# Optimization experiments

Measured on AMD Instinct MI355X. Metric: run time of the kernel, lower is better.

The kernel has to match this reference:

```python
import jax, jax.numpy as jnp
import numpy as np

C = 128          # hidden width hard-coded in DirModelToFace
EPS = 1e-5       # BatchNorm1d eps


def sparse_bmm(rows, cols, vals, x, num_rows):
    """Batched sparse @ dense: COO (rows, cols, vals) shared across batch.
    x: [B, K, c] -> [B, num_rows, c]."""
    def one(xb):
        return jax.ops.segment_sum(xb[cols] * vals[:, None], rows, num_segments=num_rows)
    return jax.vmap(one)(x)


def conv1x1_prebn(x, gamma, beta, W, b):
    # GraphConv1x1(batch_norm='pre'): BN (training stats over B*N rows) then Linear
    mean = x.mean((0, 1))
    var = x.var((0, 1))  # biased, as torch BN uses for normalization
    xh = (x - mean) * jax.lax.rsqrt(var + EPS) * gamma + beta
    return xh @ W + b


def dir_block(Di, DiA, v, f, g, be, W, b):
    # DirResNet2 (res_f=False): quaternionic Dirac message passing
    B, N, _ = v.shape
    Fn = f.shape[1]
    msg_v = sparse_bmm(*DiA, f.reshape(B, 4 * Fn, C // 4), 4 * N).reshape(B, N, C)
    x = jax.nn.elu(jnp.concatenate([v, msg_v], axis=-1))
    v_out = v + conv1x1_prebn(x, g[0], be[0], W[0], b[0])
    msg_f = sparse_bmm(*Di, v_out.reshape(B, 4 * N, C // 4), 4 * Fn).reshape(B, Fn, C)
    x = jax.nn.elu(jnp.concatenate([f, msg_f], axis=-1))
    f_out = conv1x1_prebn(x, g[1], be[1], W[1], b[1])  # no residual on f
    return v_out, f_out


def avg_block(mask, v, g, be, W, b):
    # AvgResNet2: masked global average message
    x = v
    for j in range(2):
        x = jax.nn.elu(x)
        x_avg = (mask * x).sum(1, keepdims=True) / mask.sum(1, keepdims=True)
        x = jnp.concatenate([x, jnp.broadcast_to(x_avg, x.shape)], axis=-1)
        x = conv1x1_prebn(x, g[j], be[j], W[j], b[j])
    return x + v


def setup_inputs() -> dict:
    key = jax.random.key(0)
    ks = jax.random.split(key, 10)
    B, N, Fn = 4, 12000, 24000
    nnz = 48 * Fn  # 3 vertices per face x 4x4 quaternion block
    inputs = jax.random.normal(ks[0], (B, N, 3), jnp.float32)
    mask = jnp.ones((B, N, 1), jnp.float32)
    Di_rows = jax.random.randint(ks[1], (nnz,), 0, 4 * Fn, jnp.int32)
    Di_cols = jax.random.randint(ks[2], (nnz,), 0, 4 * N, jnp.int32)
    Di_vals = jax.random.normal(ks[3], (nnz,), jnp.float32) * 0.1
    DiA_rows = jax.random.randint(ks[4], (nnz,), 0, 4 * N, jnp.int32)
    DiA_cols = jax.random.randint(ks[5], (nnz,), 0, 4 * Fn, jnp.int32)
    DiA_vals = jax.random.normal(ks[6], (nnz,), jnp.float32) * 0.1
    W1 = jax.random.normal(ks[7], (3, C), jnp.float32) / np.sqrt(3.0)
    b1 = jnp.zeros((C,), jnp.float32)
    rn_gamma = jnp.ones((16, 2, 2 * C), jnp.float32)
    rn_beta = jnp.zeros((16, 2, 2 * C), jnp.float32)
    rn_W = jax.random.normal(ks[8], (16, 2, 2 * C, C), jnp.float32) / np.sqrt(2.0 * C)
    rn_b = jnp.zeros((16, 2, C), jnp.float32)
    g2 = jnp.ones((C,), jnp.float32)
    be2 = jnp.zeros((C,), jnp.float32)
    W2 = jax.random.normal(ks[9], (C, 1), jnp.float32) / np.sqrt(1.0 * C)
    b2 = jnp.zeros((1,), jnp.float32)
    return dict(inputs=inputs, mask=mask,
                Di_rows=Di_rows, Di_cols=Di_cols, Di_vals=Di_vals,
                DiA_rows=DiA_rows, DiA_cols=DiA_cols, DiA_vals=DiA_vals,
                W1=W1, b1=b1, rn_gamma=rn_gamma, rn_beta=rn_beta, rn_W=rn_W, rn_b=rn_b,
                g2=g2, be2=be2, W2=W2, b2=b2, num_faces=24000)


def reference(inputs, mask, Di_rows, Di_cols, Di_vals, DiA_rows, DiA_cols, DiA_vals,
              W1, b1, rn_gamma, rn_beta, rn_W, rn_b, g2, be2, W2, b2, num_faces):
    B, N, _ = inputs.shape
    v = inputs @ W1 + b1                       # conv1 (batch_norm=None)
    f = jnp.zeros((B, num_faces, C), v.dtype)  # face features start at zero
    Di = (Di_rows, Di_cols, Di_vals)
    DiA = (DiA_rows, DiA_cols, DiA_vals)
    for i in range(16):
        if i % 2 == 0:
            v, f = dir_block(Di, DiA, v, f, rn_gamma[i], rn_beta[i], rn_W[i], rn_b[i])
        else:
            v = avg_block(mask, v, rn_gamma[i], rn_beta[i], rn_W[i], rn_b[i])
    x = jax.nn.elu(f)
    return conv1x1_prebn(x, g2, be2, W2, b2)   # conv2 (batch_norm='pre')
```

## Files before the change

kernel.cpp:

```cpp
#include <hip/hip_runtime.h>
#include <hip/hip_fp16.h>
#include <math.h>


#define EPS 1e-5f

typedef float floatx4 __attribute__((ext_vector_type(4)));
typedef short shortx8 __attribute__((ext_vector_type(8)));

__device__ __forceinline__ float eluf(float x) { return x > 0.f ? x : expm1f(x); }
__device__ __forceinline__ float4 elu4(float4 v) {
    v.x = eluf(v.x); v.y = eluf(v.y); v.z = eluf(v.z); v.w = eluf(v.w); return v;
}
__device__ __forceinline__ short f2bf(float x) {
    unsigned u = __builtin_bit_cast(unsigned, x);
    u = u + 0x7FFFu + ((u >> 16) & 1u);
    return (short)(u >> 16);
}
__device__ __forceinline__ float bf2f(short h) {
    unsigned u = ((unsigned)(unsigned short)h) << 16;
    return __builtin_bit_cast(float, u);
}
__device__ __forceinline__ void split2(float x, short& hi, short& lo) {
    unsigned u = __builtin_bit_cast(unsigned, x);
    hi = (short)(u >> 16);
    float r = x - bf2f(hi);
    lo = (short)(__builtin_bit_cast(unsigned, r) >> 16);
}

__global__ void conv1_kernel(const float* __restrict__ in, const float* __restrict__ W1,
                             const float* __restrict__ b1, float* __restrict__ v,
                             __half* __restrict__ vH, int N, float* __restrict__ Sout) {
    int t = threadIdx.x;
    int c = t & 127, half = t >> 7;
    int r0 = blockIdx.x * 64;
    float w0 = W1[c], w1 = W1[128 + c], w2 = W1[256 + c], bb = b1[c];
    float s1 = 0.f, s2 = 0.f;
    for (int k = 0; k < 32; ++k) {
        int r = r0 + half + 2 * k;
        float x0 = in[r * 3 + 0], x1 = in[r * 3 + 1], x2 = in[r * 3 + 2];
        float val = bb + x0 * w0 + x1 * w1 + x2 * w2;
        v[(size_t)r * 128 + c] = val;
        int b = r / N, vert = r - b * N;
        vH[(size_t)(4 * vert + (c >> 5)) * 128 + b * 32 + (c & 31)] = __float2half(val);
        float e = eluf(val);
        s1 += e; s2 += e * e;
    }
    atomicAdd(&Sout[c], s1);
    atomicAdd(&Sout[256 + c], s2);
}

__global__ void masksum_kernel(const float* __restrict__ mask, float* __restrict__ msum,
                               int N) {
    int b = blockIdx.x, t = threadIdx.x;
    float s = 0.f;
    for (int n = t; n < N; n += 256) s += mask[(size_t)b * N + n];
    for (int o = 32; o > 0; o >>= 1) s += __shfl_down(s, o);
    __shared__ float sh[4];
    if ((t & 63) == 0) sh[t >> 6] = s;
    __syncthreads();
    if (t == 0) msum[b] = sh[0] + sh[1] + sh[2] + sh[3];
}


__global__ void hist_kernel(const int* __restrict__ rows, int* __restrict__ counts) {
    int e = blockIdx.x * 256 + threadIdx.x;
    atomicAdd(&counts[rows[e]], 1);
}

__global__ void partial_kernel(const int* __restrict__ counts, int* __restrict__ partials,
                               int R) {
    int t = threadIdx.x;
    int base = blockIdx.x * 1024 + t * 4;
    int s = 0;
#pragma unroll
    for (int j = 0; j < 4; ++j) { int i = base + j; if (i < R) s += counts[i]; }
    __shared__ int sh[256];
    sh[t] = s; __syncthreads();
    for (int st = 128; st > 0; st >>= 1) {
        if (t < st) sh[t] += sh[t + st];
        __syncthreads();
    }
    if (t == 0) partials[blockIdx.x] = sh[0];
}

__global__ void scanp_kernel(int* __restrict__ partials, int* __restrict__ rowptr,
                             int P, int R, int total) {
    __shared__ int sh[256];
    int t = threadIdx.x;
    int v = (t < P) ? partials[t] : 0;
    sh[t] = v; __syncthreads();
    for (int st = 1; st < 256; st <<= 1) {
        int tmp = (t >= st) ? sh[t - st] : 0;
        __syncthreads();
        sh[t] += tmp;
        __syncthreads();
    }
    if (t < P) partials[t] = sh[t] - v;
    if (t == 0) rowptr[R] = total;
}

__global__ void apply_kernel(int* __restrict__ counts, const int* __restrict__ partials,
                             int* __restrict__ rowptr, int R) {
    int t = threadIdx.x;
    int base = blockIdx.x * 1024 + t * 4;
    int c[4]; int s = 0;
#pragma unroll
    for (int j = 0; j < 4; ++j) { int i = base + j; c[j] = (i < R) ? counts[i] : 0; s += c[j]; }
    __shared__ int sh[256];
    sh[t] = s; __syncthreads();
    for (int st = 1; st < 256; st <<= 1) {
        int tmp = (t >= st) ? sh[t - st] : 0;
        __syncthreads();
        sh[t] += tmp;
        __syncthreads();
    }
    int off = partials[blockIdx.x] + sh[t] - s;
#pragma unroll
    for (int j = 0; j < 4; ++j) {
        int i = base + j;
        if (i < R) { rowptr[i] = off; counts[i] = off; }
        off += c[j];
    }
}

__global__ void scatter_kernel(const int* __restrict__ rows, const int* __restrict__ cols,
                               const float* __restrict__ vals, int* __restrict__ fill,
                               int2* __restrict__ edges) {
    int e = blockIdx.x * 256 + threadIdx.x;
    int p = atomicAdd(&fill[rows[e]], 1);
    edges[p] = make_int2(cols[e], __float_as_int(vals[e]));
}

__global__ __launch_bounds__(1024) void spmm_csr_kernel(
    const int* __restrict__ rowptr, const int2* __restrict__ edges,
    const __half2* __restrict__ xH, float* __restrict__ y, int R4,
    float* __restrict__ Sout) {
    int t = threadIdx.x;
    int waveId = blockIdx.x * 16 + (t >> 6);
    int lane = t & 63;
    int b = lane >> 4, cp = lane & 15;
    const __half2* xb = xH + b * 16 + cp;
    size_t rs = (size_t)R4 * 32;
    __shared__ float red[256];
    if (t < 256) red[t] = 0.f;
    __syncthreads();
#pragma unroll
    for (int rr = 0; rr < 2; ++rr) {
        int r = waveId * 2 + rr;
        int e0 = rowptr[r], e1 = rowptr[r + 1];
        float ax = 0.f, ay = 0.f;
        int e = e0;
        for (; e + 4 <= e1; e += 4) {
            int2 E0 = edges[e], E1 = edges[e + 1], E2 = edges[e + 2], E3 = edges[e + 3];
            __half2 g0 = xb[(size_t)E0.x * 64];
            __half2 g1 = xb[(size_t)E1.x * 64];
            __half2 g2 = xb[(size_t)E2.x * 64];
            __half2 g3 = xb[(size_t)E3.x * 64];
            float v0 = __int_as_float(E0.y), v1 = __int_as_float(E1.y);
            float v2 = __int_as_float(E2.y), v3 = __int_as_float(E3.y);
            float2 f0 = __half22float2(g0), f1 = __half22float2(g1);
            float2 f2 = __half22float2(g2), f3 = __half22float2(g3);
            ax += v0 * f0.x; ay += v0 * f0.y;
            ax += v1 * f1.x; ay += v1 * f1.y;
            ax += v2 * f2.x; ay += v2 * f2.y;
            ax += v3 * f3.x; ay += v3 * f3.y;
        }
        for (; e < e1; ++e) {
            int2 E = edges[e];
            __half2 g = xb[(size_t)E.x * 64];
            float v = __int_as_float(E.y);
            float2 f = __half22float2(g);
            ax += v * f.x; ay += v * f.y;
        }
        *(float2*)&y[(size_t)b * rs + (size_t)r * 32 + cp * 2] = make_float2(ax, ay);
        float ea = eluf(ax), eb = eluf(ay);
        float s1a = ea, s2a = ea * ea, s1b = eb, s2b = eb * eb;
        s1a += __shfl_xor(s1a, 16); s1a += __shfl_xor(s1a, 32);
        s2a += __shfl_xor(s2a, 16); s2a += __shfl_xor(s2a, 32);
        s1b += __shfl_xor(s1b, 16); s1b += __shfl_xor(s1b, 32);
        s2b += __shfl_xor(s2b, 16); s2b += __shfl_xor(s2b, 32);
        if (lane < 16) {
            int ch = (r & 3) * 32 + cp * 2;
            atomicAdd(&red[ch], s1a);
            atomicAdd(&red[ch + 1], s1b);
            atomicAdd(&red[128 + ch], s2a);
            atomicAdd(&red[128 + ch + 1], s2b);
        }
    }
    __syncthreads();
    if (t < 128) atomicAdd(&Sout[128 + t], red[t]);
    else if (t < 256) atomicAdd(&Sout[384 + (t - 128)], red[t]);
}

__global__ void fold_kernel(const float* __restrict__ S, const float* __restrict__ gamma,
                            const float* __restrict__ beta, const float* __restrict__ W,
                            const float* __restrict__ bvec, short* __restrict__ Wh,
                            short* __restrict__ Wl, float* __restrict__ bp, float invR) {
    __shared__ float red[256];
    int o = blockIdx.x, k = threadIdx.x;
    float mean = S[k] * invR;
    float var = S[256 + k] * invR - mean * mean;
    float s = gamma[k] / sqrtf(var + EPS);
    float w = W[(size_t)k * 128 + o];
    float wp = s * w;
    short h = f2bf(wp);
    Wh[(size_t)o * 256 + k] = h;
    Wl[(size_t)o * 256 + k] = f2bf(wp - bf2f(h));
    red[k] = (beta[k] - mean * s) * w;
    __syncthreads();
    for (int st = 128; st > 0; st >>= 1) {
        if (k < st) red[k] += red[k + st];
        __syncthreads();
    }
    if (k == 0) bp[o] = bvec[o] + red[0];
}

__global__ __launch_bounds__(256) void gemm_mfma(
    const float* __restrict__ A, const float* __restrict__ Bs,
    const short* __restrict__ Wh, const short* __restrict__ Wl,
    const float* __restrict__ bp, const float* __restrict__ resid,
    float* __restrict__ out, __half* __restrict__ shadow,
    float* __restrict__ Sout, const float* __restrict__ mask,
    float* __restrict__ avgout, int rowsPerBatch, int modeB, int eluB) {
    __shared__ short Bsh[128 * 40];
    __shared__ short Bsl[128 * 40];
    const int t = threadIdx.x;
    const int lane = t & 63;
    const int wave = t >> 6;
    const int rowBase = blockIdx.x * 128 + wave * 32;
    const int m = lane & 15;
    const int kq = lane >> 4;
    floatx4 acc[2][8];
#pragma unroll
    for (int i = 0; i < 2; ++i)
#pragma unroll
        for (int j = 0; j < 8; ++j) acc[i][j] = {0.f, 0.f, 0.f, 0.f};

    const int kbEnd = (modeB == 2) ? 4 : 8;
    for (int kb = 0; kb < kbEnd; ++kb) {
        const int k0 = kb * 32 + kq * 8;
        __syncthreads();
#pragma unroll
        for (int i = 0; i < 2; ++i) {
            int idx = t + 256 * i;
            int col = idx >> 2, q = idx & 3;
            shortx8 h = *(const shortx8*)&Wh[(size_t)col * 256 + kb * 32 + q * 8];
            shortx8 l = *(const shortx8*)&Wl[(size_t)col * 256 + kb * 32 + q * 8];
            *(shortx8*)&Bsh[col * 40 + q * 8] = h;
            *(shortx8*)&Bsl[col * 40 + q * 8] = l;
        }
        shortx8 ah[2], al[2];
#pragma unroll
        for (int rg = 0; rg < 2; ++rg) {
            int row = rowBase + rg * 16 + m;
            float4 p, q;
            if (kb < 4) {
                p = elu4(*(const float4*)&A[(size_t)row * 128 + k0]);
                q = elu4(*(const float4*)&A[(size_t)row * 128 + k0 + 4]);
            } else {
                int kk = k0 - 128;
                if (modeB == 0) {
                    p = *(const float4*)&Bs[(size_t)row * 128 + kk];
                    q = *(const float4*)&Bs[(size_t)row * 128 + kk + 4];
                    if (eluB) { p = elu4(p); q = elu4(q); }
                } else {
                    int b = row / rowsPerBatch;
                    p = *(const float4*)&Bs[b * 128 + kk];
                    q = *(const float4*)&Bs[b * 128 + kk + 4];
                }
            }
            float x[8] = {p.x, p.y, p.z, p.w, q.x, q.y, q.z, q.w};
#pragma unroll
            for (int j = 0; j < 8; ++j) {
                short h, l;
                split2(x[j], h, l);
                ah[rg][j] = h;
                al[rg][j] = l;
            }
        }
        __syncthreads();
#pragma unroll
        for (int ct = 0; ct < 8; ++ct) {
            int co = (ct * 16 + m) * 40 + kq * 8;
            shortx8 bh = *(const shortx8*)&Bsh[co];
            shortx8 bl = *(const shortx8*)&Bsl[co];
#pragma unroll
            for (int rg = 0; rg < 2; ++rg) {
                acc[rg][ct] = __builtin_amdgcn_mfma_f32_16x16x32_bf16(ah[rg], bh, acc[rg][ct], 0, 0, 0);
                acc[rg][ct] = __builtin_amdgcn_mfma_f32_16x16x32_bf16(ah[rg], bl, acc[rg][ct], 0, 0, 0);
                acc[rg][ct] = __builtin_amdgcn_mfma_f32_16x16x32_bf16(al[rg], bh, acc[rg][ct], 0, 0, 0);
            }
        }
    }
    const int bBlk = (blockIdx.x * 128) / rowsPerBatch;
    float mk8[8]; int ib8[8];
    if (avgout) {
#pragma unroll
        for (int rg = 0; rg < 2; ++rg)
#pragma unroll
            for (int r = 0; r < 4; ++r) {
                int row = rowBase + rg * 16 + kq * 4 + r;
                mk8[rg * 4 + r] = mask[row];
                ib8[rg * 4 + r] = (row >= (bBlk + 1) * rowsPerBatch) ? 1 : 0;
            }
    }
    float cs1[8], cs2[8], av0[8], av1[8];
#pragma unroll
    for (int ct = 0; ct < 8; ++ct) { cs1[ct] = 0.f; cs2[ct] = 0.f; av0[ct] = 0.f; av1[ct] = 0.f; }
#pragma unroll
    for (int ct = 0; ct < 8; ++ct) {
        int col = ct * 16 + m;
        float bb = bp[col];
#pragma unroll
        for (int rg = 0; rg < 2; ++rg) {
#pragma unroll
            for (int r = 0; r < 4; ++r) {
                int row = rowBase + rg * 16 + kq * 4 + r;
                size_t o = (size_t)row * 128 + col;
                float v = acc[rg][ct][r] + bb;
                if (resid) v += resid[o];
                out[o] = v;
                if (shadow) {
                    int b = row / rowsPerBatch, vert = row - b * rowsPerBatch;
                    shadow[(size_t)(4 * vert + (col >> 5)) * 128 + b * 32 + (col & 31)] =
                        __float2half(v);
                }
                float e = eluf(v);
                cs1[ct] += e; cs2[ct] += e * e;
                if (avgout) {
                    float me = mk8[rg * 4 + r] * e;
                    if (ib8[rg * 4 + r]) av1[ct] += me; else av0[ct] += me;
                }
            }
        }
    }
    if (Sout) {
        __syncthreads();
        float* red = (float*)Bsh;
        float* redv = (float*)Bsl;
        red[t] = 0.f;
        if (avgout) redv[t] = 0.f;
        __syncthreads();
#pragma unroll
        for (int ct = 0; ct < 8; ++ct) {
            cs1[ct] += __shfl_xor(cs1[ct], 16); cs1[ct] += __shfl_xor(cs1[ct], 32);
            cs2[ct] += __shfl_xor(cs2[ct], 16); cs2[ct] += __shfl_xor(cs2[ct], 32);
            if (avgout) {
                av0[ct] += __shfl_xor(av0[ct], 16); av0[ct] += __shfl_xor(av0[ct], 32);
                av1[ct] += __shfl_xor(av1[ct], 16); av1[ct] += __shfl_xor(av1[ct], 32);
            }
        }
        if (kq == 0) {
#pragma unroll
            for (int ct = 0; ct < 8; ++ct) {
                atomicAdd(&red[ct * 16 + m], cs1[ct]);
                atomicAdd(&red[128 + ct * 16 + m], cs2[ct]);
                if (avgout) {
                    atomicAdd(&redv[ct * 16 + m], av0[ct]);
                    atomicAdd(&redv[128 + ct * 16 + m], av1[ct]);
                }
            }
        }
        __syncthreads();
        if (t < 128) atomicAdd(&Sout[t], red[t]);
        else atomicAdd(&Sout[256 + (t - 128)], red[t]);
        if (avgout) {
            int plane = t >> 7, col = t & 127;
            int b = bBlk + plane;
            if (b < 4) atomicAdd(&avgout[b * 128 + col], redv[t]);
        }
    }
}

__global__ void finalize_avg(const float* __restrict__ avgacc, const float* __restrict__ masksum,
                             float* __restrict__ avg, float* __restrict__ S, float fN) {
    int c = threadIdx.x;
    float s1 = 0.f, s2 = 0.f;
    for (int b = 0; b < 4; ++b) {
        float a = avgacc[b * 128 + c] / masksum[b];
        avg[b * 128 + c] = a;
        s1 += a; s2 += a * a;
    }
    S[128 + c] = s1 * fN;
    S[256 + 128 + c] = s2 * fN;
}

__global__ void fold_final(const float* __restrict__ S, const float* __restrict__ g2,
                           const float* __restrict__ be2, const float* __restrict__ W2,
                           const float* __restrict__ b2, float* __restrict__ W2p, float invR) {
    __shared__ float red[128];
    int c = threadIdx.x;
    float mean = S[c] * invR;
    float var = S[256 + c] * invR - mean * mean;
    float s = g2[c] / sqrtf(var + EPS);
    float w = W2[c];
    W2p[c] = s * w;
    red[c] = (be2[c] - mean * s) * w;
    __syncthreads();
    for (int st = 64; st > 0; st >>= 1) {
        if (c < st) red[c] += red[c + st];
        __syncthreads();
    }
    if (c == 0) W2p[128] = b2[0] + red[0];
}

__global__ void final_out_kernel(const float* __restrict__ f, const float* __restrict__ W2p,
                                 float* __restrict__ out) {
    int t = threadIdx.x;
    int w = t >> 6, lane = t & 63;
    int row = blockIdx.x * 4 + w;
    float a = eluf(f[(size_t)row * 128 + lane]) * W2p[lane] +
              eluf(f[(size_t)row * 128 + 64 + lane]) * W2p[64 + lane];
    for (int off = 32; off > 0; off >>= 1) a += __shfl_down(a, off);
    if (lane == 0) out[row] = a + W2p[128];
}

extern "C" void kernel_launch(void* const* d_in, const int* in_sizes, int n_in,
                              void* d_out, int out_size, void* d_ws, size_t ws_size,
                              hipStream_t stream) {
    const float* inputs = (const float*)d_in[0];
    const float* mask = (const float*)d_in[1];
    const int* Di_rows = (const int*)d_in[2];
    const int* Di_cols = (const int*)d_in[3];
    const float* Di_vals = (const float*)d_in[4];
    const int* DiA_rows = (const int*)d_in[5];
    const int* DiA_cols = (const int*)d_in[6];
    const float* DiA_vals = (const float*)d_in[7];
    const float* W1 = (const float*)d_in[8];
    const float* b1 = (const float*)d_in[9];
    const float* rn_gamma = (const float*)d_in[10];
    const float* rn_beta = (const float*)d_in[11];
    const float* rn_W = (const float*)d_in[12];
    const float* rn_b = (const float*)d_in[13];
    const float* g2 = (const float*)d_in[14];
    const float* be2 = (const float*)d_in[15];
    const float* W2 = (const float*)d_in[16];
    const float* b2 = (const float*)d_in[17];
    float* out = (float*)d_out;

    const int B = 4;
    const int BN = in_sizes[1];
    const int N = BN / B;
    const int BF = out_size;
    const int Fn = BF / B;
    const int nnz = in_sizes[2];
    const int RA = 4 * N;
    const int RD = 4 * Fn;

    float* ws = (float*)d_ws;
    size_t off = 0;
    float* vA = ws + off;  off += (size_t)BN * 128;
    float* fA = ws + off;  off += (size_t)BF * 128;
    float* msg = ws + off; off += (size_t)BF * 128;
    __half* vH = (__half*)(ws + off); off += (size_t)RA * 128 / 2;
    __half* fH = (__half*)(ws + off); off += (size_t)RD * 128 / 2;
    int* ptrA    = (int*)(ws + off);  off += (size_t)RA + 4;
    int2* edgesA = (int2*)(ws + off); off += (size_t)nnz * 2;
    int* ptrD    = (int*)(ws + off);  off += (size_t)RD + 4;
    int2* edgesD = (int2*)(ws + off); off += (size_t)nnz * 2;
    int* tmpfill = (int*)(ws + off);  off += (size_t)RD;
    int* partials = (int*)(ws + off); off += 256;
    float* Sarena = ws + off; off += 33 * 512;
    float* Aarena = ws + off; off += 16 * 512;
    float* msum = ws + off;   off += 4;
    float* avg = ws + off;    off += 512;
    short* Wh = (short*)(ws + off); off += 128 * 256 / 2;
    short* Wl = (short*)(ws + off); off += 128 * 256 / 2;
    float* bp = ws + off;  off += 128;
    float* W2p = ws + off; off += 132;

    const int eBlocks = nnz / 256;
    const int PA = (RA + 1023) / 1024;
    const int PD = (RD + 1023) / 1024;

    hipMemsetAsync(Sarena, 0, (33 * 512 + 16 * 512) * 4, stream);
    hipMemsetAsync(fA, 0, (size_t)BF * 128 * 4, stream);

    hipMemsetAsync(tmpfill, 0, (size_t)RA * 4, stream);
    hist_kernel<<<eBlocks, 256, 0, stream>>>(DiA_rows, tmpfill);
    partial_kernel<<<PA, 256, 0, stream>>>(tmpfill, partials, RA);
    scanp_kernel<<<1, 256, 0, stream>>>(partials, ptrA, PA, RA, nnz);
    apply_kernel<<<PA, 256, 0, stream>>>(tmpfill, partials, ptrA, RA);
    scatter_kernel<<<eBlocks, 256, 0, stream>>>(DiA_rows, DiA_cols, DiA_vals, tmpfill, edgesA);
    hipMemsetAsync(tmpfill, 0, (size_t)RD * 4, stream);
    hist_kernel<<<eBlocks, 256, 0, stream>>>(Di_rows, tmpfill);
    partial_kernel<<<PD, 256, 0, stream>>>(tmpfill, partials, RD);
    scanp_kernel<<<1, 256, 0, stream>>>(partials, ptrD, PD, RD, nnz);
    apply_kernel<<<PD, 256, 0, stream>>>(tmpfill, partials, ptrD, RD);
    scatter_kernel<<<eBlocks, 256, 0, stream>>>(Di_rows, Di_cols, Di_vals, tmpfill, edgesD);

    auto slot = [&](int i, int j) { return Sarena + 512 * (2 * i + j); };
    float* Sfinal = Sarena + 512 * 32;

    masksum_kernel<<<B, 256, 0, stream>>>(mask, msum, N);
    conv1_kernel<<<BN / 64, 256, 0, stream>>>(inputs, W1, b1, vA, vH, N, slot(0, 0));

    for (int i = 0; i < 15; ++i) {
        if ((i & 1) == 0) {
            const float* g0 = rn_gamma + (size_t)(i * 2 + 0) * 256;
            const float* be0 = rn_beta + (size_t)(i * 2 + 0) * 256;
            const float* Wl0 = rn_W + (size_t)(i * 2 + 0) * 256 * 128;
            const float* bl0 = rn_b + (size_t)(i * 2 + 0) * 128;
            const float* g1 = rn_gamma + (size_t)(i * 2 + 1) * 256;
            const float* be1 = rn_beta + (size_t)(i * 2 + 1) * 256;
            const float* Wl1 = rn_W + (size_t)(i * 2 + 1) * 256 * 128;
            const float* bl1 = rn_b + (size_t)(i * 2 + 1) * 128;
            float* SoutV = (i < 14) ? slot(i + 1, 0) : nullptr;
            float* avgV = (i < 14) ? (Aarena + 512 * i) : nullptr;

            if (i == 0) {
                fold_kernel<<<128, 256, 0, stream>>>(slot(0, 0), g0, be0, Wl0, bl0,
                                                     Wh, Wl, bp, 1.f / BN);
                gemm_mfma<<<BN / 128, 256, 0, stream>>>(vA, nullptr, Wh, Wl, bp, vA, vA,
                                                        vH, SoutV, mask, avgV, N, 2, 1);
            } else {
                spmm_csr_kernel<<<RA / 32, 1024, 0, stream>>>(ptrA, edgesA,
                                                              (const __half2*)fH, msg, RA,
                                                              slot(i, 0));
                fold_kernel<<<128, 256, 0, stream>>>(slot(i, 0), g0, be0, Wl0, bl0,
                                                     Wh, Wl, bp, 1.f / BN);
                gemm_mfma<<<BN / 128, 256, 0, stream>>>(vA, msg, Wh, Wl, bp, vA, vA,
                                                        vH, SoutV, mask, avgV, N, 0, 1);
            }

            spmm_csr_kernel<<<RD / 32, 1024, 0, stream>>>(ptrD, edgesD, (const __half2*)vH,
                                                          msg, RD, slot(i, 1));
            fold_kernel<<<128, 256, 0, stream>>>(slot(i, 1), g1, be1, Wl1, bl1, Wh, Wl,
                                                 bp, 1.f / BF);
            gemm_mfma<<<BF / 128, 256, 0, stream>>>(fA, msg, Wh, Wl, bp, nullptr, fA, fH,
                                                    (i < 14) ? slot(i + 2, 1) : Sfinal,
                                                    nullptr, nullptr, Fn, 0, 1);
        } else {
            for (int j = 0; j < 2; ++j) {
                const float* g = rn_gamma + (size_t)(i * 2 + j) * 256;
                const float* be = rn_beta + (size_t)(i * 2 + j) * 256;
                const float* Wlw = rn_W + (size_t)(i * 2 + j) * 256 * 128;
                const float* bl = rn_b + (size_t)(i * 2 + j) * 128;
                const float* src = (j == 0) ? vA : msg;
                float* dst = (j == 0) ? msg : vA;
                const float* resid = (j == 0) ? nullptr : vA;
                __half* shadow = (j == 0) ? nullptr : vH;
                float* Sout = (j == 0) ? slot(i, 1) : slot(i + 1, 0);
                float* avgO = (j == 0) ? (Aarena + 512 * i) : nullptr;

                float* avgacc = Aarena + 512 * (i - 1 + j);
                finalize_avg<<<1, 128, 0, stream>>>(avgacc, msum, avg, slot(i, j),
                                                    (float)N);
                fold_kernel<<<128, 256, 0, stream>>>(slot(i, j), g, be, Wlw, bl, Wh, Wl,
                                                     bp, 1.f / BN);
                gemm_mfma<<<BN / 128, 256, 0, stream>>>(src, avg, Wh, Wl, bp, resid, dst,
                                                        shadow, Sout, mask, avgO, N, 1, 0);
            }
        }
    }

    fold_final<<<1, 128, 0, stream>>>(Sfinal, g2, be2, W2, b2, W2p, 1.f / BF);
    final_out_kernel<<<BF / 4, 256, 0, stream>>>(fA, W2p, out);
}
```

Measured before the change: 4.195 ms.

## Store SpMM messages in fp16 and process two K-blocks per GEMM sync

The SpMM kernel now writes its message output as fp16 with nontemporal stores and reads edges with nontemporal loads. The BN statistics are computed from the rounded fp16 values so they match what the GEMM consumes. The GEMM decodes the fp16 message operand and stages two 32-wide K slices of weights in shared memory per barrier pair, halving the number of synchronizations. This cuts message write and read traffic and barrier overhead, at the cost of fp16 rounding on messages, more LDS and more registers, plus a separate fp32 scratch buffer for the average blocks.

```diff
diff --git a/kernel.cpp b/kernel.cpp
--- a/kernel.cpp
+++ b/kernel.cpp
@@ -7,6 +7,8 @@
 
 typedef float floatx4 __attribute__((ext_vector_type(4)));
 typedef short shortx8 __attribute__((ext_vector_type(8)));
+typedef int intx2 __attribute__((ext_vector_type(2)));
+typedef int intx4 __attribute__((ext_vector_type(4)));
 
 __device__ __forceinline__ float eluf(float x) { return x > 0.f ? x : expm1f(x); }
 __device__ __forceinline__ float4 elu4(float4 v) {
@@ -26,6 +28,9 @@
     hi = (short)(u >> 16);
     float r = x - bf2f(hi);
     lo = (short)(__builtin_bit_cast(unsigned, r) >> 16);
+}
+__device__ __forceinline__ float2 h2f(int bits) {
+    return __half22float2(__builtin_bit_cast(__half2, bits));
 }
 
 __global__ void conv1_kernel(const float* __restrict__ in, const float* __restrict__ W1,
@@ -134,13 +139,14 @@
 
 __global__ __launch_bounds__(1024) void spmm_csr_kernel(
     const int* __restrict__ rowptr, const int2* __restrict__ edges,
-    const __half2* __restrict__ xH, float* __restrict__ y, int R4,
+    const __half2* __restrict__ xH, __half* __restrict__ yH, int R4,
     float* __restrict__ Sout) {
     int t = threadIdx.x;
     int waveId = blockIdx.x * 16 + (t >> 6);
     int lane = t & 63;
     int b = lane >> 4, cp = lane & 15;
     const __half2* xb = xH + b * 16 + cp;
+    const intx2* eg = (const intx2*)edges;
     size_t rs = (size_t)R4 * 32;
     __shared__ float red[256];
     if (t < 256) red[t] = 0.f;
@@ -152,7 +158,10 @@
         float ax = 0.f, ay = 0.f;
         int e = e0;
         for (; e + 4 <= e1; e += 4) {
-            int2 E0 = edges[e], E1 = edges[e + 1], E2 = edges[e + 2], E3 = edges[e + 3];
+            intx2 E0 = __builtin_nontemporal_load(&eg[e]);
+            intx2 E1 = __builtin_nontemporal_load(&eg[e + 1]);
+            intx2 E2 = __builtin_nontemporal_load(&eg[e + 2]);
+            intx2 E3 = __builtin_nontemporal_load(&eg[e + 3]);
             __half2 g0 = xb[(size_t)E0.x * 64];
             __half2 g1 = xb[(size_t)E1.x * 64];
             __half2 g2 = xb[(size_t)E2.x * 64];
@@ -167,14 +176,17 @@
             ax += v3 * f3.x; ay += v3 * f3.y;
         }
         for (; e < e1; ++e) {
-            int2 E = edges[e];
+            intx2 E = __builtin_nontemporal_load(&eg[e]);
             __half2 g = xb[(size_t)E.x * 64];
             float v = __int_as_float(E.y);
             float2 f = __half22float2(g);
             ax += v * f.x; ay += v * f.y;
         }
-        *(float2*)&y[(size_t)b * rs + (size_t)r * 32 + cp * 2] = make_float2(ax, ay);
-        float ea = eluf(ax), eb = eluf(ay);
+        __half2 hv = __floats2half2_rn(ax, ay);
+        __builtin_nontemporal_store(__builtin_bit_cast(int, hv),
+                                    (int*)(yH + (size_t)b * rs + (size_t)r * 32 + cp * 2));
+        float2 fv = __half22float2(hv);
+        float ea = eluf(fv.x), eb = eluf(fv.y);
         float s1a = ea, s2a = ea * ea, s1b = eb, s2b = eb * eb;
         s1a += __shfl_xor(s1a, 16); s1a += __shfl_xor(s1a, 32);
         s2a += __shfl_xor(s2a, 16); s2a += __shfl_xor(s2a, 32);
@@ -217,14 +229,15 @@
 }
 
 __global__ __launch_bounds__(256) void gemm_mfma(
-    const float* __restrict__ A, const float* __restrict__ Bs,
-    const short* __restrict__ Wh, const short* __restrict__ Wl,
-    const float* __restrict__ bp, const float* __restrict__ resid,
-    float* __restrict__ out, __half* __restrict__ shadow,
-    float* __restrict__ Sout, const float* __restrict__ mask,
-    float* __restrict__ avgout, int rowsPerBatch, int modeB, int eluB) {
-    __shared__ short Bsh[128 * 40];
-    __shared__ short Bsl[128 * 40];
+    const float* __restrict__ A, const __half* __restrict__ BsH,
+    const float* __restrict__ Bsf, const short* __restrict__ Wh,
+    const short* __restrict__ Wl, const float* __restrict__ bp,
+    const float* __restrict__ resid, float* __restrict__ out,
+    __half* __restrict__ shadow, float* __restrict__ Sout,
+    const float* __restrict__ mask, float* __restrict__ avgout,
+    int rowsPerBatch, int modeB, int eluB) {
+    __shared__ short Bh2[2][128 * 40];
+    __shared__ short Bl2[2][128 * 40];
     const int t = threadIdx.x;
     const int lane = t & 63;
     const int wave = t >> 6;
@@ -237,59 +250,72 @@
 #pragma unroll
         for (int j = 0; j < 8; ++j) acc[i][j] = {0.f, 0.f, 0.f, 0.f};
 
-    const int kbEnd = (modeB == 2) ? 4 : 8;
-    for (int kb = 0; kb < kbEnd; ++kb) {
-        const int k0 = kb * 32 + kq * 8;
-        __syncthreads();
-#pragma unroll
-        for (int i = 0; i < 2; ++i) {
-            int idx = t + 256 * i;
-            int col = idx >> 2, q = idx & 3;
-            shortx8 h = *(const shortx8*)&Wh[(size_t)col * 256 + kb * 32 + q * 8];
-            shortx8 l = *(const shortx8*)&Wl[(size_t)col * 256 + kb * 32 + q * 8];
-            *(shortx8*)&Bsh[col * 40 + q * 8] = h;
-            *(shortx8*)&Bsl[col * 40 + q * 8] = l;
-        }
-        shortx8 ah[2], al[2];
-#pragma unroll
-        for (int rg = 0; rg < 2; ++rg) {
-            int row = rowBase + rg * 16 + m;
-            float4 p, q;
-            if (kb < 4) {
-                p = elu4(*(const float4*)&A[(size_t)row * 128 + k0]);
-                q = elu4(*(const float4*)&A[(size_t)row * 128 + k0 + 4]);
-            } else {
-                int kk = k0 - 128;
-                if (modeB == 0) {
-                    p = *(const float4*)&Bs[(size_t)row * 128 + kk];
-                    q = *(const float4*)&Bs[(size_t)row * 128 + kk + 4];
-                    if (eluB) { p = elu4(p); q = elu4(q); }
+    const int kb2End = (modeB == 2) ? 2 : 4;
+    for (int kb2 = 0; kb2 < kb2End; ++kb2) {
+        __syncthreads();
+#pragma unroll
+        for (int s = 0; s < 2; ++s) {
+            int kb = kb2 * 2 + s;
+#pragma unroll
+            for (int i = 0; i < 2; ++i) {
+                int idx = t + 256 * i;
+                int col = idx >> 2, q = idx & 3;
+                shortx8 h = *(const shortx8*)&Wh[(size_t)col * 256 + kb * 32 + q * 8];
+                shortx8 l = *(const shortx8*)&Wl[(size_t)col * 256 + kb * 32 + q * 8];
+                *(shortx8*)&Bh2[s][col * 40 + q * 8] = h;
+                *(shortx8*)&Bl2[s][col * 40 + q * 8] = l;
+            }
+        }
+        shortx8 ah[2][2], al[2][2];
+#pragma unroll
+        for (int s = 0; s < 2; ++s) {
+            int kb = kb2 * 2 + s;
+            int k0 = kb * 32 + kq * 8;
+#pragma unroll
+            for (int rg = 0; rg < 2; ++rg) {
+                int row = rowBase + rg * 16 + m;
+                float4 p, q;
+                if (kb < 4) {
+                    p = elu4(*(const float4*)&A[(size_t)row * 128 + k0]);
+                    q = elu4(*(const float4*)&A[(size_t)row * 128 + k0 + 4]);
                 } else {
-                    int b = row / rowsPerBatch;
-                    p = *(const float4*)&Bs[b * 128 + kk];
-                    q = *(const float4*)&Bs[b * 128 + kk + 4];
+                    int kk = k0 - 128;
+                    if (modeB == 0) {
+                        intx4 raw = *(const intx4*)&BsH[(size_t)row * 128 + kk];
+                        float2 f0 = h2f(raw.x), f1 = h2f(raw.y);
+                        float2 f2 = h2f(raw.z), f3 = h2f(raw.w);
+                        p = elu4(make_float4(f0.x, f0.y, f1.x, f1.y));
+                        q = elu4(make_float4(f2.x, f2.y, f3.x, f3.y));
+                    } else {
+                        int b = row / rowsPerBatch;
+                        p = *(const float4*)&Bsf[b * 128 + kk];
+                        q = *(const float4*)&Bsf[b * 128 + kk + 4];
+                    }
                 }
-            }
-            float x[8] = {p.x, p.y, p.z, p.w, q.x, q.y, q.z, q.w};
-#pragma unroll
-            for (int j = 0; j < 8; ++j) {
-                short h, l;
-                split2(x[j], h, l);
-                ah[rg][j] = h;
-                al[rg][j] = l;
+                float x[8] = {p.x, p.y, p.z, p.w, q.x, q.y, q.z, q.w};
+#pragma unroll
+                for (int j = 0; j < 8; ++j) {
+                    short h, l;
+                    split2(x[j], h, l);
+                    ah[s][rg][j] = h;
+                    al[s][rg][j] = l;
+                }
             }
         }
         __syncthreads();
 #pragma unroll
         for (int ct = 0; ct < 8; ++ct) {
             int co = (ct * 16 + m) * 40 + kq * 8;
-            shortx8 bh = *(const shortx8*)&Bsh[co];
-            shortx8 bl = *(const shortx8*)&Bsl[co];
-#pragma unroll
-            for (int rg = 0; rg < 2; ++rg) {
-                acc[rg][ct] = __builtin_amdgcn_mfma_f32_16x16x32_bf16(ah[rg], bh, acc[rg][ct], 0, 0, 0);
-                acc[rg][ct] = __builtin_amdgcn_mfma_f32_16x16x32_bf16(ah[rg], bl, acc[rg][ct], 0, 0, 0);
-                acc[rg][ct] = __builtin_amdgcn_mfma_f32_16x16x32_bf16(al[rg], bh, acc[rg][ct], 0, 0, 0);
+#pragma unroll
+            for (int s = 0; s < 2; ++s) {
+                shortx8 bh = *(const shortx8*)&Bh2[s][co];
+                shortx8 bl = *(const shortx8*)&Bl2[s][co];
+#pragma unroll
+                for (int rg = 0; rg < 2; ++rg) {
+                    acc[rg][ct] = __builtin_amdgcn_mfma_f32_16x16x32_bf16(ah[s][rg], bh, acc[rg][ct], 0, 0, 0);
+                    acc[rg][ct] = __builtin_amdgcn_mfma_f32_16x16x32_bf16(ah[s][rg], bl, acc[rg][ct], 0, 0, 0);
+                    acc[rg][ct] = __builtin_amdgcn_mfma_f32_16x16x32_bf16(al[s][rg], bh, acc[rg][ct], 0, 0, 0);
+                }
             }
         }
     }
@@ -337,8 +363,8 @@
     }
     if (Sout) {
         __syncthreads();
-        float* red = (float*)Bsh;
-        float* redv = (float*)Bsl;
+        float* red = (float*)Bh2;
+        float* redv = (float*)Bl2;
         red[t] = 0.f;
         if (avgout) redv[t] = 0.f;
         __syncthreads();
@@ -452,7 +478,8 @@
     size_t off = 0;
     float* vA = ws + off;  off += (size_t)BN * 128;
     float* fA = ws + off;  off += (size_t)BF * 128;
-    float* msg = ws + off; off += (size_t)BF * 128;
+    float* xT = ws + off;  off += (size_t)BN * 128;
+    __half* msgH = (__half*)(ws + off); off += (size_t)BF * 128 / 2;
     __half* vH = (__half*)(ws + off); off += (size_t)RA * 128 / 2;
     __half* fH = (__half*)(ws + off); off += (size_t)RD * 128 / 2;
     int* ptrA    = (int*)(ws + off);  off += (size_t)RA + 4;
@@ -512,23 +539,26 @@
             if (i == 0) {
                 fold_kernel<<<128, 256, 0, stream>>>(slot(0, 0), g0, be0, Wl0, bl0,
                                                      Wh, Wl, bp, 1.f / BN);
-                gemm_mfma<<<BN / 128, 256, 0, stream>>>(vA, nullptr, Wh, Wl, bp, vA, vA,
-                                                        vH, SoutV, mask, avgV, N, 2, 1);
+                gemm_mfma<<<BN / 128, 256, 0, stream>>>(vA, nullptr, nullptr, Wh, Wl, bp,
+                                                        vA, vA, vH, SoutV, mask, avgV,
+                                                        N, 2, 1);
             } else {
                 spmm_csr_kernel<<<RA / 32, 1024, 0, stream>>>(ptrA, edgesA,
-                                                              (const __half2*)fH, msg, RA,
+                                                              (const __half2*)fH, msgH, RA,
                                                               slot(i, 0));
                 fold_kernel<<<128, 256, 0, stream>>>(slot(i, 0), g0, be0, Wl0, bl0,
                                                      Wh, Wl, bp, 1.f / BN);
-                gemm_mfma<<<BN / 128, 256, 0, stream>>>(vA, msg, Wh, Wl, bp, vA, vA,
-                                                        vH, SoutV, mask, avgV, N, 0, 1);
+                gemm_mfma<<<BN / 128, 256, 0, stream>>>(vA, msgH, nullptr, Wh, Wl, bp,
+                                                        vA, vA, vH, SoutV, mask, avgV,
+                                                        N, 0, 1);
             }
 
             spmm_csr_kernel<<<RD / 32, 1024, 0, stream>>>(ptrD, edgesD, (const __half2*)vH,
-                                                          msg, RD, slot(i, 1));
+                                                          msgH, RD, slot(i, 1));
             fold_kernel<<<128, 256, 0, stream>>>(slot(i, 1), g1, be1, Wl1, bl1, Wh, Wl,
                                                  bp, 1.f / BF);
-            gemm_mfma<<<BF / 128, 256, 0, stream>>>(fA, msg, Wh, Wl, bp, nullptr, fA, fH,
+            gemm_mfma<<<BF / 128, 256, 0, stream>>>(fA, msgH, nullptr, Wh, Wl, bp, nullptr,
+                                                    fA, fH,
                                                     (i < 14) ? slot(i + 2, 1) : Sfinal,
                                                     nullptr, nullptr, Fn, 0, 1);
         } else {
@@ -537,8 +567,8 @@
                 const float* be = rn_beta + (size_t)(i * 2 + j) * 256;
                 const float* Wlw = rn_W + (size_t)(i * 2 + j) * 256 * 128;
                 const float* bl = rn_b + (size_t)(i * 2 + j) * 128;
-                const float* src = (j == 0) ? vA : msg;
-                float* dst = (j == 0) ? msg : vA;
+                const float* src = (j == 0) ? vA : xT;
+                float* dst = (j == 0) ? xT : vA;
                 const float* resid = (j == 0) ? nullptr : vA;
                 __half* shadow = (j == 0) ? nullptr : vH;
                 float* Sout = (j == 0) ? slot(i, 1) : slot(i + 1, 0);
@@ -549,8 +579,9 @@
                                                     (float)N);
                 fold_kernel<<<128, 256, 0, stream>>>(slot(i, j), g, be, Wlw, bl, Wh, Wl,
                                                      bp, 1.f / BN);
-                gemm_mfma<<<BN / 128, 256, 0, stream>>>(src, avg, Wh, Wl, bp, resid, dst,
-                                                        shadow, Sout, mask, avgO, N, 1, 0);
+                gemm_mfma<<<BN / 128, 256, 0, stream>>>(src, nullptr, avg, Wh, Wl, bp,
+                                                        resid, dst, shadow, Sout, mask,
+                                                        avgO, N, 1, 0);
             }
         }
     }
```

New measurement: 4.265 ms. Within noise of the previous version (+1.7%).
